# Kernel tuning notes

Measured on AMD Instinct MI355X. Metric: run time of the kernel, lower is better.

## Reference

```python
import jax, jax.numpy as jnp
import numpy as np
from jax import lax


def build_scharr_filter(size):
    assert size % 2 == 1
    c = size // 2
    wx = np.zeros((size, size), np.float32)
    wy = np.zeros((size, size), np.float32)
    for i in range(size):
        for j in range(size):
            dx = j - c
            dy = i - c
            wx[i, j] = dx * (3 if abs(dx) == 1 else 10 if dx == 0 else 1)
            wy[i, j] = dy * (3 if abs(dy) == 1 else 10 if dy == 0 else 1)
    return jnp.asarray(wx), jnp.asarray(wy)


SIZE = 3


def build_normals(xyz, size=SIZE):
    # xyz: (B, 3, H, W). Depthwise conv: for each of x,y,z apply scharr_x and scharr_y.
    kx, ky = build_scharr_filter(size)
    # kernel (6,1,s,s): [Sxx, Sxy, Syx, Syy, Szx, Szy] via feature_group_count=3
    kernel = jnp.stack([kx, ky, kx, ky, kx, ky])[:, None]
    p = size // 2
    g = lax.conv_general_dilated(
        xyz, kernel, window_strides=(1, 1), padding=[(p, p), (p, p)],
        dimension_numbers=("NCHW", "OIHW", "NCHW"), feature_group_count=3)
    Sxx, Sxy = g[:, 0:1], g[:, 1:2]
    Syx, Syy = g[:, 2:3], g[:, 3:4]
    Szx, Szy = g[:, 4:5], g[:, 5:6]
    normal = jnp.concatenate([
        Syx * Szy - Szx * Syy,
        Szx * Sxy - Szy * Sxx,
        Sxx * Syy - Syx * Sxy,
    ], axis=1)
    n = jnp.linalg.norm(normal, axis=1, keepdims=True) + jnp.float32(1e-10)
    return normal / n


def setup_inputs() -> dict:
    key = jax.random.key(0)
    k1, k2, k3 = jax.random.split(key, 3)
    B, H, W = 16, 384, 1280
    xyz_pred = jax.random.normal(k1, (B, 3, H, W), dtype=jnp.float32)
    xyz_gt = jax.random.normal(k2, (B, 3, H, W), dtype=jnp.float32)
    mask = jax.random.uniform(k3, (B, 1, H, W), dtype=jnp.float32)
    return {"xyz_pred": xyz_pred, "xyz_gt": xyz_gt, "mask": mask}


def reference(xyz_pred, xyz_gt, mask):
    normals_pred = build_normals(xyz_pred)
    normals_gt = build_normals(xyz_gt)
    loss = jnp.sum(mask * jnp.abs(normals_pred - normals_gt))
    denom = jnp.sum(mask)
    return loss / denom
```

## Files before the change

kernel.cpp:

```cpp
#include <hip/hip_runtime.h>

#define BB  16
#define HH  384
#define WW  1280
#define TPB 256
#define ROWS 16
#define NSLOT 64

__device__ __forceinline__ void load_row3(const float* __restrict__ plane, int i, int j,
                                          float& a, float& b, float& c) {
    const float* row = plane + (size_t)i * WW;
    a = (j > 0)      ? row[j - 1] : 0.f;
    b = row[j];
    c = (j < WW - 1) ? row[j + 1] : 0.f;
}

__global__ __launch_bounds__(TPB)
void NormalLoss_44478681317469_main(const float* __restrict__ pred,
                                    const float* __restrict__ gt,
                                    const float* __restrict__ mask,
                                    double* __restrict__ acc)
{
    const int j  = blockIdx.x * TPB + threadIdx.x;
    const int r0 = blockIdx.y * ROWS;
    const int b  = blockIdx.z;

    const float* pl[6];
#pragma unroll
    for (int c = 0; c < 3; ++c) {
        pl[c]     = pred + (size_t)(b * 3 + c) * HH * WW;
        pl[3 + c] = gt   + (size_t)(b * 3 + c) * HH * WW;
    }
    const float* mpl = mask + (size_t)b * HH * WW;

    float Dm1[6], D0[6], Tm1[6], T0[6];
    float Ra[6], Rb[6], Rc[6];

#pragma unroll
    for (int c = 0; c < 6; ++c) {
        if (r0 > 0) {
            float a, bb, cc; load_row3(pl[c], r0 - 1, j, a, bb, cc);
            Dm1[c] = cc - a; Tm1[c] = a + bb + cc;
        } else { Dm1[c] = 0.f; Tm1[c] = 0.f; }
        {
            float a, bb, cc; load_row3(pl[c], r0, j, a, bb, cc);
            D0[c] = cc - a; T0[c] = a + bb + cc;
        }
    }

#pragma unroll
    for (int c = 0; c < 6; ++c)
        load_row3(pl[c], r0 + 1, j, Ra[c], Rb[c], Rc[c]);
    float mrow = mpl[(size_t)r0 * WW + j];

    float lsum = 0.f, msum = 0.f;

#pragma unroll 2
    for (int k = 0; k < ROWS; ++k) {
        const int i = r0 + k;

        float Dp1[6], Tp1[6];
#pragma unroll
        for (int c = 0; c < 6; ++c) {
            Dp1[c] = Rc[c] - Ra[c];
            Tp1[c] = Ra[c] + Rb[c] + Rc[c];
        }
        float m = mrow;

        if (i + 2 < HH) {
#pragma unroll
            for (int c = 0; c < 6; ++c) load_row3(pl[c], i + 2, j, Ra[c], Rb[c], Rc[c]);
        } else {
#pragma unroll
            for (int c = 0; c < 6; ++c) { Ra[c] = 0.f; Rb[c] = 0.f; Rc[c] = 0.f; }
        }
        if (k + 1 < ROWS) mrow = mpl[(size_t)(i + 1) * WW + j];

        float gx[6], gy[6];
#pragma unroll
        for (int c = 0; c < 6; ++c) {
            gx[c] = Dm1[c] + D0[c] + Dp1[c];
            gy[c] = Tp1[c] - Tm1[c];
        }

        float n0p = gx[1] * gy[2] - gx[2] * gy[1];
        float n1p = gx[2] * gy[0] - gx[0] * gy[2];
        float n2p = gx[0] * gy[1] - gx[1] * gy[0];
        float n0g = gx[4] * gy[5] - gx[5] * gy[4];
        float n1g = gx[5] * gy[3] - gx[3] * gy[5];
        float n2g = gx[3] * gy[4] - gx[4] * gy[3];

        float sp = n0p * n0p + n1p * n1p + n2p * n2p;
        float sg = n0g * n0g + n1g * n1g + n2g * n2g;
        float ip = (sp > 1e-20f) ? __builtin_amdgcn_rsqf(sp) : 0.f;
        float ig = (sg > 1e-20f) ? __builtin_amdgcn_rsqf(sg) : 0.f;

        float d0 = fabsf(n0p * ip - n0g * ig);
        float d1 = fabsf(n1p * ip - n1g * ig);
        float d2 = fabsf(n2p * ip - n2g * ig);

        lsum += m * (d0 + d1 + d2);
        msum += m;

#pragma unroll
        for (int c = 0; c < 6; ++c) {
            Dm1[c] = D0[c]; D0[c] = Dp1[c];
            Tm1[c] = T0[c]; T0[c] = Tp1[c];
        }
    }

#pragma unroll
    for (int off = 32; off > 0; off >>= 1) {
        lsum += __shfl_down(lsum, off, 64);
        msum += __shfl_down(msum, off, 64);
    }
    __shared__ float sL[TPB / 64], sM[TPB / 64];
    const int lane = threadIdx.x & 63;
    const int wid  = threadIdx.x >> 6;
    if (lane == 0) { sL[wid] = lsum; sM[wid] = msum; }
    __syncthreads();
    if (threadIdx.x == 0) {
        float L = 0.f, M = 0.f;
#pragma unroll
        for (int w = 0; w < TPB / 64; ++w) { L += sL[w]; M += sM[w]; }
        const int linear = (blockIdx.z * gridDim.y + blockIdx.y) * gridDim.x + blockIdx.x;
        double* slot = acc + (size_t)(linear & (NSLOT - 1)) * 8;
        atomicAdd(&slot[0], (double)L);
        atomicAdd(&slot[1], (double)M);
    }
}

__global__ void NormalLoss_44478681317469_final(const double* __restrict__ acc,
                                                float* __restrict__ out)
{
    const int t = threadIdx.x;
    double L = acc[(size_t)t * 8 + 0];
    double M = acc[(size_t)t * 8 + 1];
#pragma unroll
    for (int off = 32; off > 0; off >>= 1) {
        L += __shfl_down(L, off, 64);
        M += __shfl_down(M, off, 64);
    }
    if (t == 0) out[0] = (float)(L / M);
}

extern "C" void kernel_launch(void* const* d_in, const int* in_sizes, int n_in,
                              void* d_out, int out_size, void* d_ws, size_t ws_size,
                              hipStream_t stream)
{
    const float* pred = (const float*)d_in[0];
    const float* gt   = (const float*)d_in[1];
    const float* mask = (const float*)d_in[2];
    double* acc = (double*)d_ws;

    hipMemsetAsync(acc, 0, NSLOT * 8 * sizeof(double), stream);

    dim3 grid(WW / TPB, HH / ROWS, BB);
    NormalLoss_44478681317469_main<<<grid, dim3(TPB), 0, stream>>>(pred, gt, mask, acc);
    NormalLoss_44478681317469_final<<<1, 64, 0, stream>>>(acc, (float*)d_out);
}
```

Baseline: 237.7 us.

## Replace neighbor column loads with wavefront shuffles using 64-lane overlapping tiles

Each lane now loads a single column per row and obtains left/right neighbors via cross-lane shuffles, with blocks of one wavefront covering 62 output columns plus two halo lanes. This cuts global/cache load instructions per element roughly threefold and removes the shared-memory block reduction. In exchange it wastes two lanes per wave, uses misaligned row starts, and issues more blocks and atomics.

New measurement: 242.7 us. 2.1% more time.

```diff
diff --git a/kernel.cpp b/kernel.cpp
--- a/kernel.cpp
+++ b/kernel.cpp
@@ -3,27 +3,52 @@
 #define BB  16
 #define HH  384
 #define WW  1280
-#define TPB 256
 #define ROWS 16
+#define CPW 62
+#define NGROUP 21
 #define NSLOT 64
 
-__device__ __forceinline__ void load_row3(const float* __restrict__ plane, int i, int j,
-                                          float& a, float& b, float& c) {
-    const float* row = plane + (size_t)i * WW;
-    a = (j > 0)      ? row[j - 1] : 0.f;
-    b = row[j];
-    c = (j < WW - 1) ? row[j + 1] : 0.f;
+
+__device__ __forceinline__ float load_col(const float* __restrict__ plane,
+                                          int i, int j, bool jok) {
+    return jok ? plane[(size_t)i * WW + j] : 0.f;
 }
 
-__global__ __launch_bounds__(TPB)
+__device__ __forceinline__ void taps(float v, float& D, float& T) {
+    const float lft = __shfl_up(v, 1, 64);
+    const float rgt = __shfl_down(v, 1, 64);
+    D = rgt - lft;
+    T = lft + v + rgt;
+}
+
+__device__ __forceinline__ float normal_absdiff(const float* gx, const float* gy)
+{
+    float n0p = gx[1] * gy[2] - gx[2] * gy[1];
+    float n1p = gx[2] * gy[0] - gx[0] * gy[2];
+    float n2p = gx[0] * gy[1] - gx[1] * gy[0];
+    float n0g = gx[4] * gy[5] - gx[5] * gy[4];
+    float n1g = gx[5] * gy[3] - gx[3] * gy[5];
+    float n2g = gx[3] * gy[4] - gx[4] * gy[3];
+    float sp = n0p * n0p + n1p * n1p + n2p * n2p;
+    float sg = n0g * n0g + n1g * n1g + n2g * n2g;
+    float ip = (sp > 1e-20f) ? __builtin_amdgcn_rsqf(sp) : 0.f;
+    float ig = (sg > 1e-20f) ? __builtin_amdgcn_rsqf(sg) : 0.f;
+    return fabsf(n0p * ip - n0g * ig) + fabsf(n1p * ip - n1g * ig)
+         + fabsf(n2p * ip - n2g * ig);
+}
+
+__global__ __launch_bounds__(64)
 void NormalLoss_44478681317469_main(const float* __restrict__ pred,
                                     const float* __restrict__ gt,
                                     const float* __restrict__ mask,
                                     double* __restrict__ acc)
 {
-    const int j  = blockIdx.x * TPB + threadIdx.x;
-    const int r0 = blockIdx.y * ROWS;
-    const int b  = blockIdx.z;
+    const int lane = threadIdx.x;
+    const int j    = blockIdx.x * CPW - 1 + lane;
+    const bool jok = (unsigned)j < WW;
+    const int r0   = blockIdx.y * ROWS;
+    const int b    = blockIdx.z;
+    const bool out_ok = (lane >= 1) && (lane <= CPW) && jok;
 
     const float* pl[6];
 #pragma unroll
@@ -34,24 +59,24 @@
     const float* mpl = mask + (size_t)b * HH * WW;
 
     float Dm1[6], D0[6], Tm1[6], T0[6];
-    float Ra[6], Rb[6], Rc[6];
+    float Rv[6];
 
 #pragma unroll
     for (int c = 0; c < 6; ++c) {
         if (r0 > 0) {
-            float a, bb, cc; load_row3(pl[c], r0 - 1, j, a, bb, cc);
-            Dm1[c] = cc - a; Tm1[c] = a + bb + cc;
+            float v = load_col(pl[c], r0 - 1, j, jok);
+            taps(v, Dm1[c], Tm1[c]);
         } else { Dm1[c] = 0.f; Tm1[c] = 0.f; }
         {
-            float a, bb, cc; load_row3(pl[c], r0, j, a, bb, cc);
-            D0[c] = cc - a; T0[c] = a + bb + cc;
+            float v = load_col(pl[c], r0, j, jok);
+            taps(v, D0[c], T0[c]);
         }
     }
 
 #pragma unroll
     for (int c = 0; c < 6; ++c)
-        load_row3(pl[c], r0 + 1, j, Ra[c], Rb[c], Rc[c]);
-    float mrow = mpl[(size_t)r0 * WW + j];
+        Rv[c] = load_col(pl[c], r0 + 1, j, jok);
+    float mrow = jok ? mpl[(size_t)r0 * WW + j] : 0.f;
 
     float lsum = 0.f, msum = 0.f;
 
@@ -61,20 +86,17 @@
 
         float Dp1[6], Tp1[6];
 #pragma unroll
-        for (int c = 0; c < 6; ++c) {
-            Dp1[c] = Rc[c] - Ra[c];
-            Tp1[c] = Ra[c] + Rb[c] + Rc[c];
-        }
-        float m = mrow;
+        for (int c = 0; c < 6; ++c) taps(Rv[c], Dp1[c], Tp1[c]);
+        const float m = out_ok ? mrow : 0.f;
 
         if (i + 2 < HH) {
 #pragma unroll
-            for (int c = 0; c < 6; ++c) load_row3(pl[c], i + 2, j, Ra[c], Rb[c], Rc[c]);
+            for (int c = 0; c < 6; ++c) Rv[c] = load_col(pl[c], i + 2, j, jok);
         } else {
 #pragma unroll
-            for (int c = 0; c < 6; ++c) { Ra[c] = 0.f; Rb[c] = 0.f; Rc[c] = 0.f; }
+            for (int c = 0; c < 6; ++c) Rv[c] = 0.f;
         }
-        if (k + 1 < ROWS) mrow = mpl[(size_t)(i + 1) * WW + j];
+        if (k + 1 < ROWS) mrow = jok ? mpl[(size_t)(i + 1) * WW + j] : 0.f;
 
         float gx[6], gy[6];
 #pragma unroll
@@ -83,23 +105,8 @@
             gy[c] = Tp1[c] - Tm1[c];
         }
 
-        float n0p = gx[1] * gy[2] - gx[2] * gy[1];
-        float n1p = gx[2] * gy[0] - gx[0] * gy[2];
-        float n2p = gx[0] * gy[1] - gx[1] * gy[0];
-        float n0g = gx[4] * gy[5] - gx[5] * gy[4];
-        float n1g = gx[5] * gy[3] - gx[3] * gy[5];
-        float n2g = gx[3] * gy[4] - gx[4] * gy[3];
-
-        float sp = n0p * n0p + n1p * n1p + n2p * n2p;
-        float sg = n0g * n0g + n1g * n1g + n2g * n2g;
-        float ip = (sp > 1e-20f) ? __builtin_amdgcn_rsqf(sp) : 0.f;
-        float ig = (sg > 1e-20f) ? __builtin_amdgcn_rsqf(sg) : 0.f;
-
-        float d0 = fabsf(n0p * ip - n0g * ig);
-        float d1 = fabsf(n1p * ip - n1g * ig);
-        float d2 = fabsf(n2p * ip - n2g * ig);
-
-        lsum += m * (d0 + d1 + d2);
+        const float d = normal_absdiff(gx, gy);
+        lsum += m * d;
         msum += m;
 
 #pragma unroll
@@ -114,19 +121,11 @@
         lsum += __shfl_down(lsum, off, 64);
         msum += __shfl_down(msum, off, 64);
     }
-    __shared__ float sL[TPB / 64], sM[TPB / 64];
-    const int lane = threadIdx.x & 63;
-    const int wid  = threadIdx.x >> 6;
-    if (lane == 0) { sL[wid] = lsum; sM[wid] = msum; }
-    __syncthreads();
-    if (threadIdx.x == 0) {
-        float L = 0.f, M = 0.f;
-#pragma unroll
-        for (int w = 0; w < TPB / 64; ++w) { L += sL[w]; M += sM[w]; }
+    if (lane == 0) {
         const int linear = (blockIdx.z * gridDim.y + blockIdx.y) * gridDim.x + blockIdx.x;
         double* slot = acc + (size_t)(linear & (NSLOT - 1)) * 8;
-        atomicAdd(&slot[0], (double)L);
-        atomicAdd(&slot[1], (double)M);
+        atomicAdd(&slot[0], (double)lsum);
+        atomicAdd(&slot[1], (double)msum);
     }
 }
 
@@ -155,7 +154,7 @@
 
     hipMemsetAsync(acc, 0, NSLOT * 8 * sizeof(double), stream);
 
-    dim3 grid(WW / TPB, HH / ROWS, BB);
-    NormalLoss_44478681317469_main<<<grid, dim3(TPB), 0, stream>>>(pred, gt, mask, acc);
+    dim3 grid(NGROUP, HH / ROWS, BB);
+    NormalLoss_44478681317469_main<<<grid, dim3(64), 0, stream>>>(pred, gt, mask, acc);
     NormalLoss_44478681317469_final<<<1, 64, 0, stream>>>(acc, (float*)d_out);
 }
```
